# Kernel tuning notes

Hardware: AMD Instinct MI355X
Metric: run time of the kernel (lower is better)

Reference implementation:

```python
import jax, jax.numpy as jnp
import numpy as np

N_V, N_H, T, B = 1024, 512, 128, 256


def setup_inputs() -> dict:
    key = jax.random.key(0)
    k = jax.random.split(key, 3)
    v_data = (jax.random.uniform(k[0], (N_V, T, B)) < 0.5).astype(jnp.float32)  # binary visibles
    W = 0.01 * jax.random.normal(k[1], (N_H, N_V), jnp.float32)
    U = 0.01 * jax.random.normal(k[2], (N_H, N_H), jnp.float32)
    b_h = jnp.zeros((N_H,), jnp.float32)
    b_init = jnp.zeros((N_H,), jnp.float32)
    b_v = jnp.zeros((N_V,), jnp.float32)
    return {"v_data": v_data, "W": W, "U": U, "b_h": b_h, "b_init": b_init,
            "b_v": b_v, "CDk": 2}


def _sample_r_over_time(v, W, U, b_h, b_init):
    # v: (V,T,B) -> r: (H,T,B). Sequential mean-field recurrence over T
    # (RTRBM._sample_r_given_v_over_time: t=0 uses b_init and U=0, t>0 uses U,b_h).
    Wv = jnp.einsum('hv,vtb->thb', W, v)  # (T,H,B)
    r0 = jax.nn.sigmoid(Wv[0] + b_init[:, None])

    def step(r_lag, wv_t):
        r_t = jax.nn.sigmoid(wv_t + U @ r_lag + b_h[:, None])
        return r_t, r_t

    _, rs = jax.lax.scan(step, r0, Wv[1:])
    r = jnp.concatenate([r0[None], rs], axis=0)  # (T,H,B)
    return jnp.transpose(r, (1, 0, 2))  # (H,T,B)


def _parallel_r(v, r_lagged, W, U, b_h, b_init):
    # RTRBM._parallel_sample_r_h_given_v probabilities; v:(V,T,B), r_lagged:(H,T,B)
    r0 = jax.nn.sigmoid(jnp.einsum('hv,vb->hb', W, v[:, 0]) + b_init[:, None])
    rr = jax.nn.sigmoid(jnp.einsum('hv,vtb->htb', W, v[:, 1:])
                        + jnp.einsum('hr,rtb->htb', U, r_lagged[:, :-1])
                        + b_h[:, None, None])
    return jnp.concatenate([r0[:, None], rr], axis=1)  # (H,T,B)


def reference(v_data, W, U, b_h, b_init, b_v, CDk):
    key = jax.random.key(42)
    r_data = _sample_r_over_time(v_data, W, U, b_h, b_init)
    key, sk = jax.random.split(key)
    h_model = jax.random.bernoulli(sk, _parallel_r(v_data, r_data, W, U, b_h, b_init)).astype(v_data.dtype)
    for _ in range(CDk - 1):  # CD-k Gibbs chain (CDk is a concrete Python int)
        key, k1, k2 = jax.random.split(key, 3)
        v_prob = jax.nn.sigmoid(jnp.einsum('hv,htb->vtb', W, h_model) + b_v[:, None, None])
        v_model = jax.random.bernoulli(k1, v_prob).astype(v_data.dtype)
        h_model = jax.random.bernoulli(k2, _parallel_r(v_model, r_data, W, U, b_h, b_init)).astype(v_data.dtype)
    key, kf = jax.random.split(key)
    v_model = jax.random.bernoulli(
        kf, jax.nn.sigmoid(jnp.einsum('hv,htb->vtb', W, h_model) + b_v[:, None, None])
    ).astype(v_data.dtype)
    return (v_model, r_data)
```

## Files before the change

kernel.cpp:

```cpp
#include <hip/hip_runtime.h>
#include <hip/hip_bf16.h>
#include <stdint.h>

typedef unsigned long long u64;
typedef uint32_t u32;
typedef __attribute__((ext_vector_type(8))) short bf16x8;
typedef __attribute__((ext_vector_type(4))) float f32x4;

#define NV 1024
#define NH 512
#define TT 128
#define BB 256
#define TBsz (TT*BB)
#define HTBsz (NH*TBsz)
#define VTBsz (NV*TBsz)
#define NWV (NV/64)
#define NWH (NH/64)
#define QCAP 1048576u
#define DELTA 5e-4

__host__ __device__ inline void tf2x32(uint32_t k0, uint32_t k1,
                                       uint32_t x0, uint32_t x1,
                                       uint32_t& o0, uint32_t& o1) {
  const uint32_t ks2 = k0 ^ k1 ^ 0x1BD11BDAu;
#define ROTL(x,d) (((x)<<(d))|((x)>>(32-(d))))
#define RND(r) { x0 += x1; x1 = ROTL(x1,r); x1 ^= x0; }
  x0 += k0;  x1 += k1;
  RND(13) RND(15) RND(26) RND(6)
  x0 += k1;  x1 += ks2 + 1u;
  RND(17) RND(29) RND(16) RND(24)
  x0 += ks2; x1 += k0 + 2u;
  RND(13) RND(15) RND(26) RND(6)
  x0 += k0;  x1 += k1 + 3u;
  RND(17) RND(29) RND(16) RND(24)
  x0 += k1;  x1 += ks2 + 4u;
  RND(13) RND(15) RND(26) RND(6)
  x0 += ks2; x1 += k0 + 5u;
  o0 = x0; o1 = x1;
#undef RND
#undef ROTL
}

__device__ inline double tf_uniform64(uint32_t k0, uint32_t k1, uint32_t i) {
  uint32_t o0, o1;
  tf2x32(k0, k1, 0u, i, o0, o1);
  uint32_t bits = o0 ^ o1;
  uint32_t fb = (bits >> 9) | 0x3f800000u;
  float f = __uint_as_float(fb) - 1.0f;
  return (double)f;
}

__device__ inline double sigmoid64(double x) { return 1.0 / (1.0 + exp(-x)); }

__global__ __launch_bounds__(256) void kcvt(const float* __restrict__ s,
                                            double* __restrict__ d, int n) {
  int i = blockIdx.x * 256 + threadIdx.x;
  if (i < n) d[i] = (double)s[i];
}

__global__ __launch_bounds__(256) void kprepU(const float* __restrict__ U,
                                              float4* __restrict__ UB) {
  int i = blockIdx.x * 256 + threadIdx.x;
  int r4 = i / NH;
  int h  = i % NH;
  const float* __restrict__ p = U + (size_t)h*NH + r4*4;
  UB[i] = make_float4(p[0], p[1], p[2], p[3]);
}

__global__ __launch_bounds__(256) void kprepUT(const float* __restrict__ U,
                                               float* __restrict__ UT) {
  int i = blockIdx.x * 256 + threadIdx.x;
  int r = i / NH;
  int h = i % NH;
  UT[i] = U[(size_t)h*NH + r];
}

__global__ __launch_bounds__(256) void kprepA(const float* __restrict__ W,
                                              ushort* __restrict__ A1,
                                              ushort* __restrict__ A2) {
  int idx = blockIdx.x * 256 + threadIdx.x;
  int i    = idx & 7;
  int lane = (idx >> 3) & 63;
  int ks   = (idx >> 9) & 15;
  int vt   = idx >> 13;
  int h = ks*32 + ((lane >> 4) << 3) + i;
  int v = vt*16 + (lane & 15);
  float w = W[(size_t)h*NV + v];
  __hip_bfloat16 b1 = __float2bfloat16(w);
  float r = w - __bfloat162float(b1);
  __hip_bfloat16 b2 = __float2bfloat16(r);
  A1[idx] = *reinterpret_cast<ushort*>(&b1);
  A2[idx] = *reinterpret_cast<ushort*>(&b2);
}

__global__ __launch_bounds__(256) void kpack_f32(const float* __restrict__ in,
                                                 u64* __restrict__ out) {
  int tb = blockIdx.x * 256 + threadIdx.x;
  for (int w = 0; w < NWV; ++w) {
    u64 m = 0;
    #pragma unroll 8
    for (int j = 0; j < 64; ++j)
      m |= (u64)(in[(size_t)(w*64 + j)*TBsz + tb] != 0.0f ? 1 : 0) << j;
    out[(size_t)tb*NWV + w] = m;
  }
}

__global__ __launch_bounds__(256) void kWv(const u64* __restrict__ vb,
                                           const double* __restrict__ W64,
                                           double* __restrict__ WvT) {
  const int HM = 8;
  int t  = blockIdx.x / (NH/HM);
  int h0 = (blockIdx.x % (NH/HM)) * HM;
  int tb = t*BB + threadIdx.x;
  u64 m[NWV];
  #pragma unroll
  for (int w = 0; w < NWV; ++w) m[w] = vb[(size_t)tb*NWV + w];
  double acc[HM];
  #pragma unroll
  for (int i = 0; i < HM; ++i) acc[i] = 0.0;
  const double2* __restrict__ W2 = (const double2*)W64;
  for (int w = 0; w < NWV; ++w) {
    u64 mw = m[w];
    #pragma unroll 8
    for (int j2 = 0; j2 < 32; ++j2) {
      double bd0 = (double)((unsigned)((mw >> (2*j2+0)) & 1ull));
      double bd1 = (double)((unsigned)((mw >> (2*j2+1)) & 1ull));
      int vi = w*32 + j2;
      #pragma unroll
      for (int i = 0; i < HM; ++i) {
        double2 wv = W2[(size_t)(h0+i)*(NV/2) + vi];
        acc[i] = fma(bd0, wv.x, acc[i]);
        acc[i] = fma(bd1, wv.y, acc[i]);
      }
    }
  }
  #pragma unroll
  for (int i = 0; i < HM; ++i)
    WvT[(size_t)tb*NH + h0 + i] = acc[i];
}

__global__ __launch_bounds__(512) void krecur(const double* __restrict__ WvT,
                                              const float4* __restrict__ UB,
                                              const float* __restrict__ bh,
                                              const float* __restrict__ binit,
                                              double* __restrict__ rT) {
  __shared__ double rA[2][NH];
  const int b = blockIdx.x;
  const int h = threadIdx.x;
  const double bhd = (double)bh[h];
  float4 ureg[32];
  #pragma unroll
  for (int i = 0; i < 32; ++i) ureg[i] = UB[(size_t)i*NH + h];
  double p = sigmoid64(WvT[(size_t)b*NH + h] + (double)binit[h]);
  rA[0][h] = p;
  rT[(size_t)b*NH + h] = p;
  __syncthreads();
  int cur = 0;
  for (int t = 1; t < TT; ++t) {
    double acc = WvT[((size_t)t*BB + b)*NH + h];
    double a0=0, a1=0, a2=0, a3=0;
    const double2* __restrict__ rA2 = (const double2*)rA[cur];
    #pragma unroll 8
    for (int r = 0; r < 128; r += 4) {
      float4 u4 = ureg[r >> 2];
      double2 q01 = rA2[(r>>1)+0];
      double2 q23 = rA2[(r>>1)+1];
      a0 = fma((double)u4.x, q01.x, a0);
      a1 = fma((double)u4.y, q01.y, a1);
      a2 = fma((double)u4.z, q23.x, a2);
      a3 = fma((double)u4.w, q23.y, a3);
    }
    #pragma unroll 4
    for (int r = 128; r < NH; r += 4) {
      float4 u4 = UB[(size_t)(r >> 2)*NH + h];
      double2 q01 = rA2[(r>>1)+0];
      double2 q23 = rA2[(r>>1)+1];
      a0 = fma((double)u4.x, q01.x, a0);
      a1 = fma((double)u4.y, q01.y, a1);
      a2 = fma((double)u4.z, q23.x, a2);
      a3 = fma((double)u4.w, q23.y, a3);
    }
    p = sigmoid64((acc + ((a0+a1)+(a2+a3))) + bhd);
    rA[cur ^ 1][h] = p;
    rT[((size_t)t*BB + b)*NH + h] = p;
    __syncthreads();
    cur ^= 1;
  }
}

__global__ __launch_bounds__(256) void ktrans_s(const double* __restrict__ rT,
                                                float* __restrict__ out_r,
                                                uint8_t* __restrict__ hbytes,
                                                u32 k0, u32 k1) {
  __shared__ double lds[32][33];
  int t  = blockIdx.x;
  int h0 = blockIdx.y * 32;
  int b0 = blockIdx.z * 32;
  int tx = threadIdx.x & 31;
  int ty = threadIdx.x >> 5;
  #pragma unroll
  for (int i = 0; i < 4; ++i) {
    int row = ty*4 + i;
    lds[row][tx] = rT[((size_t)t*BB + b0 + row)*NH + h0 + tx];
  }
  __syncthreads();
  #pragma unroll
  for (int i = 0; i < 4; ++i) {
    int row = ty*4 + i;
    out_r[(size_t)(h0+row)*TBsz + (size_t)t*BB + b0 + tx] = (float)lds[tx][row];
  }
  if (threadIdx.x < 128) {
    int tbr = threadIdx.x >> 2;
    int bix = threadIdx.x & 3;
    int tb  = t*BB + b0 + tbr;
    unsigned byte = 0;
    #pragma unroll
    for (int j = 0; j < 8; ++j) {
      int hrel = bix*8 + j;
      double p = lds[tbr][hrel];
      double u = tf_uniform64(k0, k1, (u32)((h0 + hrel)*TBsz + tb));
      byte |= (u < p) ? (1u << j) : 0u;
    }
    hbytes[(size_t)tb*(NH/8) + (h0 >> 3) + bix] = (uint8_t)byte;
  }
}

__global__ __launch_bounds__(256) void kvisM(
    const ushort* __restrict__ A1, const ushort* __restrict__ A2,
    const float* __restrict__ bv, const u64* __restrict__ hbits,
    u64* __restrict__ vbits, float* __restrict__ vf,
    u32* __restrict__ queue, u32* __restrict__ cnt, u32 k0, u32 k1) {
  __shared__ ushort Blds[64*512];
  int nblk = blockIdx.x & 511;
  int vblk = blockIdx.x >> 9;
  int tb0 = nblk * 64, v0 = vblk * 64;
  int tid = threadIdx.x;
  {
    int c = tid >> 2, seg = tid & 3;
    const u64* hp = hbits + (size_t)(tb0 + c)*NWH + seg*2;
    #pragma unroll
    for (int half = 0; half < 2; ++half) {
      u64 mm = hp[half];
      int kbase = seg*128 + half*64;
      #pragma unroll
      for (int j2 = 0; j2 < 32; ++j2) {
        int k = kbase + 2*j2;
        u32 val = (u32)((mm >> (2*j2)) & 1ull) * 0x3F80u
                | (u32)((mm >> (2*j2+1)) & 1ull) * 0x3F800000u;
        int blk = (k >> 3) ^ (c & 7);
        *(u32*)&Blds[c*512 + (blk << 3) + (k & 7)] = val;
      }
    }
  }
  __syncthreads();
  int wv = tid >> 6, l = tid & 63;
  int wr = wv >> 1, wc = wv & 1;
  f32x4 acc[2][2];
  #pragma unroll
  for (int m = 0; m < 2; ++m)
    #pragma unroll
    for (int n = 0; n < 2; ++n) acc[m][n] = (f32x4){0.f,0.f,0.f,0.f};
  for (int ks = 0; ks < 16; ++ks) {
    bf16x8 bf[2];
    #pragma unroll
    for (int n = 0; n < 2; ++n) {
      int col = wc*32 + n*16 + (l & 15);
      int k = ks*32 + ((l >> 4) << 3);
      int blk = (k >> 3) ^ (col & 7);
      bf[n] = *(const bf16x8*)&Blds[col*512 + (blk << 3)];
    }
    #pragma unroll
    for (int m = 0; m < 2; ++m) {
      int vt = vblk*4 + wr*2 + m;
      size_t abase = (((size_t)vt*16 + ks)*64 + l)*8;
      bf16x8 a1 = *(const bf16x8*)&A1[abase];
      bf16x8 a2 = *(const bf16x8*)&A2[abase];
      #pragma unroll
      for (int n = 0; n < 2; ++n) {
        acc[m][n] = __builtin_amdgcn_mfma_f32_16x16x32_bf16(a1, bf[n], acc[m][n], 0,0,0);
        acc[m][n] = __builtin_amdgcn_mfma_f32_16x16x32_bf16(a2, bf[n], acc[m][n], 0,0,0);
      }
    }
  }
  u64 mask[2] = {0, 0};
  int coln[2];
  #pragma unroll
  for (int n = 0; n < 2; ++n) {
    int col = wc*32 + n*16 + (l & 15);
    coln[n] = col;
    int tb = tb0 + col;
    #pragma unroll
    for (int m = 0; m < 2; ++m) {
      #pragma unroll
      for (int r = 0; r < 4; ++r) {
        int vrel = wr*32 + m*16 + ((l >> 4) << 2) + r;
        int v = v0 + vrel;
        float p = 1.f / (1.f + __expf(-(acc[m][n][r] + bv[v])));
        size_t o = (size_t)v*TBsz + tb;
        double u = tf_uniform64(k0, k1, (u32)o);
        double diff = (double)p - u;
        unsigned smp = diff > 0.0 ? 1u : 0u;
        if (fabs(diff) < DELTA) {
          u32 s = atomicAdd(cnt, 1u);
          if (s < QCAP) queue[s] = (u32)o;
        }
        if (smp) mask[n] |= 1ull << vrel;
        if (vf) vf[o] = (float)smp;
      }
    }
  }
  if (vbits) {
    __syncthreads();
    u64* sbits = (u64*)Blds;
    if (tid < 64) sbits[tid] = 0;
    __syncthreads();
    atomicOr(&sbits[coln[0]], mask[0]);
    atomicOr(&sbits[coln[1]], mask[1]);
    __syncthreads();
    if (tid < 64)
      vbits[(size_t)(tb0 + tid)*NWV + (v0 >> 6)] = sbits[tid];
  }
}

__global__ __launch_bounds__(256) void kvis_fix(
    const float* __restrict__ W, const float* __restrict__ bv,
    const u64* __restrict__ hbits, u64* __restrict__ fixbits,
    float* __restrict__ vf, const u32* __restrict__ queue,
    const u32* __restrict__ cnt, u32 k0, u32 k1) {
  u32 n = *cnt; if (n > QCAP) n = QCAP;
  for (u32 q = blockIdx.x*256 + threadIdx.x; q < n; q += gridDim.x*256) {
    u32 o = queue[q];
    u32 v = o / TBsz, tb = o % TBsz;
    double a0=0, a1=0, a2=0, a3=0;
    for (int w = 0; w < NWH; ++w) {
      u64 mw = hbits[(size_t)tb*NWH + w];
      for (int j = 0; j < 64; j += 4) {
        if ((mw >> (j+0)) & 1ull) a0 += (double)W[(size_t)(w*64+j+0)*NV + v];
        if ((mw >> (j+1)) & 1ull) a1 += (double)W[(size_t)(w*64+j+1)*NV + v];
        if ((mw >> (j+2)) & 1ull) a2 += (double)W[(size_t)(w*64+j+2)*NV + v];
        if ((mw >> (j+3)) & 1ull) a3 += (double)W[(size_t)(w*64+j+3)*NV + v];
      }
    }
    double p = sigmoid64(((a0+a1)+(a2+a3)) + (double)bv[v]);
    double u = tf_uniform64(k0, k1, o);
    unsigned smp = (u < p) ? 1u : 0u;
    if (vf) vf[o] = (float)smp;
    if (fixbits) {
      size_t wi = (size_t)tb*NWV + (v >> 6);
      unsigned bit = v & 63u;
      unsigned cur = (unsigned)((fixbits[wi] >> bit) & 1ull);
      if (cur != smp) atomicXor(&fixbits[wi], 1ull << bit);
    }
  }
}

__global__ __launch_bounds__(256) void khid32(
    const u64* __restrict__ vbits, const float* __restrict__ W,
    const float* __restrict__ UT, const float* __restrict__ bh,
    const float* __restrict__ binit, const float* __restrict__ r32,
    uint8_t* __restrict__ hbytes, u32* __restrict__ queue,
    u32* __restrict__ cnt, u32 k0, u32 k1) {
  const int HM = 8;
  int t  = blockIdx.x / (NH/HM);
  int h0 = (blockIdx.x % (NH/HM)) * HM;
  int tb = t*BB + threadIdx.x;
  u64 m[NWV];
  #pragma unroll
  for (int w = 0; w < NWV; ++w) m[w] = vbits[(size_t)tb*NWV + w];
  float acc[HM];
  #pragma unroll
  for (int i = 0; i < HM; ++i) acc[i] = 0.f;
  const float4* __restrict__ W4 = (const float4*)W;
  for (int w = 0; w < NWV; ++w) {
    u64 mw = m[w];
    #pragma unroll 4
    for (int j4 = 0; j4 < 16; ++j4) {
      float bd0 = (float)((u32)((mw >> (4*j4+0)) & 1ull));
      float bd1 = (float)((u32)((mw >> (4*j4+1)) & 1ull));
      float bd2 = (float)((u32)((mw >> (4*j4+2)) & 1ull));
      float bd3 = (float)((u32)((mw >> (4*j4+3)) & 1ull));
      int vi = w*16 + j4;
      #pragma unroll
      for (int i = 0; i < HM; ++i) {
        float4 wv = W4[(size_t)(h0+i)*(NV/4) + vi];
        acc[i] = fmaf(bd0, wv.x, acc[i]);
        acc[i] = fmaf(bd1, wv.y, acc[i]);
        acc[i] = fmaf(bd2, wv.z, acc[i]);
        acc[i] = fmaf(bd3, wv.w, acc[i]);
      }
    }
  }
  if (t > 0) {
    const float* __restrict__ rp = r32 + (size_t)(t-1)*BB + threadIdx.x;
    const float4* __restrict__ UT4 = (const float4*)UT;
    #pragma unroll 4
    for (int r = 0; r < NH; ++r) {
      float rv = rp[(size_t)r*TBsz];
      float4 ua = UT4[(size_t)r*(NH/4) + (h0 >> 2) + 0];
      float4 ub = UT4[(size_t)r*(NH/4) + (h0 >> 2) + 1];
      acc[0] = fmaf(ua.x, rv, acc[0]);
      acc[1] = fmaf(ua.y, rv, acc[1]);
      acc[2] = fmaf(ua.z, rv, acc[2]);
      acc[3] = fmaf(ua.w, rv, acc[3]);
      acc[4] = fmaf(ub.x, rv, acc[4]);
      acc[5] = fmaf(ub.y, rv, acc[5]);
      acc[6] = fmaf(ub.z, rv, acc[6]);
      acc[7] = fmaf(ub.w, rv, acc[7]);
    }
    #pragma unroll
    for (int i = 0; i < HM; ++i) acc[i] += bh[h0+i];
  } else {
    #pragma unroll
    for (int i = 0; i < HM; ++i) acc[i] += binit[h0+i];
  }
  unsigned byte = 0;
  #pragma unroll
  for (int i = 0; i < HM; ++i) {
    float p = 1.f / (1.f + __expf(-acc[i]));
    size_t o = (size_t)(h0+i)*TBsz + tb;
    double u = tf_uniform64(k0, k1, (u32)o);
    double diff = (double)p - u;
    unsigned smp = diff > 0.0 ? 1u : 0u;
    if (fabs(diff) < DELTA) {
      u32 s = atomicAdd(cnt, 1u);
      if (s < QCAP) queue[s] = (u32)o;
    }
    byte |= smp << i;
  }
  hbytes[(size_t)tb*(NH/8) + (h0 >> 3)] = (uint8_t)byte;
}

__global__ __launch_bounds__(256) void khid_fix(
    const u64* __restrict__ vbits, const float* __restrict__ W,
    const double* __restrict__ U64, const float* __restrict__ bh,
    const float* __restrict__ binit, const double* __restrict__ rT,
    u64* __restrict__ fixbits, const u32* __restrict__ queue,
    const u32* __restrict__ cnt, u32 k0, u32 k1) {
  u32 n = *cnt; if (n > QCAP) n = QCAP;
  for (u32 q = blockIdx.x*256 + threadIdx.x; q < n; q += gridDim.x*256) {
    u32 o = queue[q];
    u32 h = o / TBsz, tb = o % TBsz;
    u32 t = tb / BB, b = tb % BB;
    double a0=0, a1=0, a2=0, a3=0;
    for (int w = 0; w < NWV; ++w) {
      u64 mw = vbits[(size_t)tb*NWV + w];
      for (int j = 0; j < 64; j += 4) {
        if ((mw >> (j+0)) & 1ull) a0 += (double)W[(size_t)h*NV + w*64+j+0];
        if ((mw >> (j+1)) & 1ull) a1 += (double)W[(size_t)h*NV + w*64+j+1];
        if ((mw >> (j+2)) & 1ull) a2 += (double)W[(size_t)h*NV + w*64+j+2];
        if ((mw >> (j+3)) & 1ull) a3 += (double)W[(size_t)h*NV + w*64+j+3];
      }
    }
    double logit = (a0+a1) + (a2+a3);
    if (t > 0) {
      const double* __restrict__ rp = rT + ((size_t)(t-1)*BB + b)*NH;
      const double* __restrict__ Ur = U64 + (size_t)h*NH;
      double u0=0, u1=0, u2=0, u3=0;
      for (int r = 0; r < NH; r += 4) {
        u0 = fma(Ur[r+0], rp[r+0], u0);
        u1 = fma(Ur[r+1], rp[r+1], u1);
        u2 = fma(Ur[r+2], rp[r+2], u2);
        u3 = fma(Ur[r+3], rp[r+3], u3);
      }
      logit = (logit + ((u0+u1)+(u2+u3))) + (double)bh[h];
    } else {
      logit += (double)binit[h];
    }
    double p = sigmoid64(logit);
    double u = tf_uniform64(k0, k1, o);
    unsigned smp = (u < p) ? 1u : 0u;
    size_t wi = (size_t)tb*NWH + (h >> 6);
    unsigned bit = h & 63u;
    unsigned cur = (unsigned)((fixbits[wi] >> bit) & 1ull);
    if (cur != smp) atomicXor(&fixbits[wi], 1ull << bit);
  }
}

extern "C" void kernel_launch(void* const* d_in, const int* in_sizes, int n_in,
                              void* d_out, int out_size, void* d_ws, size_t ws_size,
                              hipStream_t stream) {
  const float* vd    = (const float*)d_in[0];
  const float* W     = (const float*)d_in[1];
  const float* U     = (const float*)d_in[2];
  const float* bh    = (const float*)d_in[3];
  const float* binit = (const float*)d_in[4];
  const float* bv    = (const float*)d_in[5];

  float* out_v = (float*)d_out;
  float* out_r = (float*)d_out + VTBsz;
  double* WvT = (double*)d_out;

  char* w = (char*)d_ws;
  double* rT    = (double*)w;  w += (size_t)HTBsz*8;
  u64* vdbits   = (u64*)w;     w += (size_t)TBsz*NWV*8;
  u64* v1bits   = (u64*)w;     w += (size_t)TBsz*NWV*8;
  u64* h1bits   = (u64*)w;     w += (size_t)TBsz*NWH*8;
  u64* h2bits   = (u64*)w;     w += (size_t)TBsz*NWH*8;
  double* W64   = (double*)w;  w += (size_t)NH*NV*8;
  double* U64   = (double*)w;  w += (size_t)NH*NH*8;
  float4* UB    = (float4*)w;  w += (size_t)NH*NH*4;
  float* UT     = (float*)w;   w += (size_t)NH*NH*4;
  ushort* A1    = (ushort*)w;  w += (size_t)NH*NV*2;
  ushort* A2    = (ushort*)w;  w += (size_t)NH*NV*2;
  u32* q0       = (u32*)w;     w += (size_t)QCAP*4;
  u32* q1       = (u32*)w;     w += (size_t)QCAP*4;
  u32* q2       = (u32*)w;     w += (size_t)QCAP*4;
  u32* cnt      = (u32*)w;     w += 256;
  (void)ws_size; (void)in_sizes; (void)n_in; (void)out_size;

  uint32_t ka0,ka1, sk0,sk1;
  tf2x32(0u,42u, 0u,0u, ka0,ka1);
  tf2x32(0u,42u, 0u,1u, sk0,sk1);
  uint32_t kb0,kb1, k10,k11, k20,k21;
  tf2x32(ka0,ka1, 0u,0u, kb0,kb1);
  tf2x32(ka0,ka1, 0u,1u, k10,k11);
  tf2x32(ka0,ka1, 0u,2u, k20,k21);
  uint32_t kc0,kc1, kf0,kf1;
  tf2x32(kb0,kb1, 0u,0u, kc0,kc1);
  tf2x32(kb0,kb1, 0u,1u, kf0,kf1);

  hipMemsetAsync(cnt, 0, 3*sizeof(u32), stream);

  kcvt<<<(NH*NV+255)/256, 256, 0, stream>>>(W, W64, NH*NV);
  kcvt<<<(NH*NH+255)/256, 256, 0, stream>>>(U, U64, NH*NH);
  kprepU<<<(NH*NH/4)/256, 256, 0, stream>>>(U, UB);
  kprepUT<<<(NH*NH)/256, 256, 0, stream>>>(U, UT);
  kprepA<<<(NH*NV)/256, 256, 0, stream>>>(W, A1, A2);
  kpack_f32<<<TBsz/256, 256, 0, stream>>>(vd, vdbits);

  kWv<<<TT*(NH/8), 256, 0, stream>>>(vdbits, W64, WvT);

  krecur<<<BB, NH, 0, stream>>>(WvT, UB, bh, binit, rT);

  ktrans_s<<<dim3(TT, NH/32, BB/32), 256, 0, stream>>>(rT, out_r,
                                                       (uint8_t*)h1bits, sk0, sk1);

  kvisM<<<16*512, 256, 0, stream>>>(A1, A2, bv, h1bits, v1bits, nullptr,
                                    q0, cnt+0, k10, k11);
  kvis_fix<<<128, 256, 0, stream>>>(W, bv, h1bits, v1bits, nullptr,
                                    q0, cnt+0, k10, k11);

  khid32<<<TT*(NH/8), 256, 0, stream>>>(v1bits, W, UT, bh, binit, out_r,
                                        (uint8_t*)h2bits, q1, cnt+1, k20, k21);
  khid_fix<<<128, 256, 0, stream>>>(v1bits, W, U64, bh, binit, rT,
                                    h2bits, q1, cnt+1, k20, k21);

  kvisM<<<16*512, 256, 0, stream>>>(A1, A2, bv, h2bits, nullptr, out_v,
                                    q2, cnt+2, kf0, kf1);
  kvis_fix<<<128, 256, 0, stream>>>(W, bv, h2bits, nullptr, out_v,
                                    q2, cnt+2, kf0, kf1);
}
```

Before: 5.709 ms.

## Compute second hidden sampling pass with bf16 split-precision MFMA GEMM

```diff
diff --git a/kernel.cpp b/kernel.cpp
--- a/kernel.cpp
+++ b/kernel.cpp
@@ -67,14 +67,6 @@
   UB[i] = make_float4(p[0], p[1], p[2], p[3]);
 }
 
-__global__ __launch_bounds__(256) void kprepUT(const float* __restrict__ U,
-                                               float* __restrict__ UT) {
-  int i = blockIdx.x * 256 + threadIdx.x;
-  int r = i / NH;
-  int h = i % NH;
-  UT[i] = U[(size_t)h*NH + r];
-}
-
 __global__ __launch_bounds__(256) void kprepA(const float* __restrict__ W,
                                               ushort* __restrict__ A1,
                                               ushort* __restrict__ A2) {
@@ -93,6 +85,42 @@
   A2[idx] = *reinterpret_cast<ushort*>(&b2);
 }
 
+__global__ __launch_bounds__(256) void kprepAW(const float* __restrict__ W,
+                                               ushort* __restrict__ AW1,
+                                               ushort* __restrict__ AW2) {
+  int idx = blockIdx.x * 256 + threadIdx.x;
+  int i    = idx & 7;
+  int lane = (idx >> 3) & 63;
+  int kt   = (idx >> 9) & 31;
+  int ht   = idx >> 14;
+  int h = ht*16 + (lane & 15);
+  int v = kt*32 + ((lane >> 4) << 3) + i;
+  float w = W[(size_t)h*NV + v];
+  __hip_bfloat16 b1 = __float2bfloat16(w);
+  float r = w - __bfloat162float(b1);
+  __hip_bfloat16 b2 = __float2bfloat16(r);
+  AW1[idx] = *reinterpret_cast<ushort*>(&b1);
+  AW2[idx] = *reinterpret_cast<ushort*>(&b2);
+}
+
+__global__ __launch_bounds__(256) void kprepAU(const float* __restrict__ U,
+                                               ushort* __restrict__ AU1,
+                                               ushort* __restrict__ AU2) {
+  int idx = blockIdx.x * 256 + threadIdx.x;
+  int i    = idx & 7;
+  int lane = (idx >> 3) & 63;
+  int kt   = (idx >> 9) & 15;
+  int ht   = idx >> 13;
+  int h = ht*16 + (lane & 15);
+  int r = kt*32 + ((lane >> 4) << 3) + i;
+  float u = U[(size_t)h*NH + r];
+  __hip_bfloat16 b1 = __float2bfloat16(u);
+  float rs = u - __bfloat162float(b1);
+  __hip_bfloat16 b2 = __float2bfloat16(rs);
+  AU1[idx] = *reinterpret_cast<ushort*>(&b1);
+  AU2[idx] = *reinterpret_cast<ushort*>(&b2);
+}
+
 __global__ __launch_bounds__(256) void kpack_f32(const float* __restrict__ in,
                                                  u64* __restrict__ out) {
   int tb = blockIdx.x * 256 + threadIdx.x;
@@ -148,9 +176,6 @@
   const int b = blockIdx.x;
   const int h = threadIdx.x;
   const double bhd = (double)bh[h];
-  float4 ureg[32];
-  #pragma unroll
-  for (int i = 0; i < 32; ++i) ureg[i] = UB[(size_t)i*NH + h];
   double p = sigmoid64(WvT[(size_t)b*NH + h] + (double)binit[h]);
   rA[0][h] = p;
   rT[(size_t)b*NH + h] = p;
@@ -160,18 +185,8 @@
     double acc = WvT[((size_t)t*BB + b)*NH + h];
     double a0=0, a1=0, a2=0, a3=0;
     const double2* __restrict__ rA2 = (const double2*)rA[cur];
-    #pragma unroll 8
-    for (int r = 0; r < 128; r += 4) {
-      float4 u4 = ureg[r >> 2];
-      double2 q01 = rA2[(r>>1)+0];
-      double2 q23 = rA2[(r>>1)+1];
-      a0 = fma((double)u4.x, q01.x, a0);
-      a1 = fma((double)u4.y, q01.y, a1);
-      a2 = fma((double)u4.z, q23.x, a2);
-      a3 = fma((double)u4.w, q23.y, a3);
-    }
     #pragma unroll 4
-    for (int r = 128; r < NH; r += 4) {
+    for (int r = 0; r < NH; r += 4) {
       float4 u4 = UB[(size_t)(r >> 2)*NH + h];
       double2 q01 = rA2[(r>>1)+0];
       double2 q23 = rA2[(r>>1)+1];
@@ -320,6 +335,159 @@
     if (tid < 64)
       vbits[(size_t)(tb0 + tid)*NWV + (v0 >> 6)] = sbits[tid];
   }
+}
+
+__global__ __launch_bounds__(256) void khidM(
+    const ushort* __restrict__ AW1, const ushort* __restrict__ AW2,
+    const ushort* __restrict__ AU1, const ushort* __restrict__ AU2,
+    const float* __restrict__ bh, const float* __restrict__ binit,
+    const u64* __restrict__ vbits, const float* __restrict__ r32,
+    u64* __restrict__ h2bits, u32* __restrict__ queue,
+    u32* __restrict__ cnt, u32 k0, u32 k1) {
+  __shared__ ushort Blds[64*512];
+  int nblk = blockIdx.x & 511;
+  int hblk = blockIdx.x >> 9;
+  int tb0 = nblk * 64, h0 = hblk * 64;
+  int t = tb0 >> 8;
+  int tid = threadIdx.x;
+  int wv = tid >> 6, l = tid & 63;
+  int wr = wv >> 1, wc = wv & 1;
+  f32x4 acc[2][2];
+  #pragma unroll
+  for (int m = 0; m < 2; ++m)
+    #pragma unroll
+    for (int n = 0; n < 2; ++n) acc[m][n] = (f32x4){0.f,0.f,0.f,0.f};
+
+  for (int q = 0; q < 2; ++q) {
+    {
+      int c = tid >> 2, seg = tid & 3;
+      const u64* vp = vbits + (size_t)(tb0 + c)*NWV + q*8 + seg*2;
+      #pragma unroll
+      for (int half = 0; half < 2; ++half) {
+        u64 mm = vp[half];
+        int kbase = seg*128 + half*64;
+        #pragma unroll
+        for (int j2 = 0; j2 < 32; ++j2) {
+          int k = kbase + 2*j2;
+          u32 val = (u32)((mm >> (2*j2)) & 1ull) * 0x3F80u
+                  | (u32)((mm >> (2*j2+1)) & 1ull) * 0x3F800000u;
+          int blk = (k >> 3) ^ (c & 7);
+          *(u32*)&Blds[c*512 + (blk << 3) + (k & 7)] = val;
+        }
+      }
+    }
+    __syncthreads();
+    for (int ks = 0; ks < 16; ++ks) {
+      int kt = q*16 + ks;
+      bf16x8 bf[2];
+      #pragma unroll
+      for (int n = 0; n < 2; ++n) {
+        int col = wc*32 + n*16 + (l & 15);
+        int k = ks*32 + ((l >> 4) << 3);
+        int blk = (k >> 3) ^ (col & 7);
+        bf[n] = *(const bf16x8*)&Blds[col*512 + (blk << 3)];
+      }
+      #pragma unroll
+      for (int m = 0; m < 2; ++m) {
+        int ht = hblk*4 + wr*2 + m;
+        size_t abase = (((size_t)ht*32 + kt)*64 + l)*8;
+        bf16x8 a1 = *(const bf16x8*)&AW1[abase];
+        bf16x8 a2 = *(const bf16x8*)&AW2[abase];
+        #pragma unroll
+        for (int n = 0; n < 2; ++n) {
+          acc[m][n] = __builtin_amdgcn_mfma_f32_16x16x32_bf16(a1, bf[n], acc[m][n], 0,0,0);
+          acc[m][n] = __builtin_amdgcn_mfma_f32_16x16x32_bf16(a2, bf[n], acc[m][n], 0,0,0);
+        }
+      }
+    }
+    __syncthreads();
+  }
+
+  if (t > 0) {
+    int tbl0 = tb0 - 256;
+    for (int pl = 0; pl < 2; ++pl) {
+      {
+        int c = tid >> 2, rseg = tid & 3;
+        const float* rp = r32 + tbl0 + c;
+        for (int rr = 0; rr < 128; ++rr) {
+          int r = rseg*128 + rr;
+          float x = rp[(size_t)r*TBsz];
+          __hip_bfloat16 b1 = __float2bfloat16(x);
+          ushort ub;
+          if (pl == 0) {
+            ub = *reinterpret_cast<ushort*>(&b1);
+          } else {
+            float res = x - __bfloat162float(b1);
+            __hip_bfloat16 b2 = __float2bfloat16(res);
+            ub = *reinterpret_cast<ushort*>(&b2);
+          }
+          int blk = (r >> 3) ^ (c & 7);
+          Blds[c*512 + (blk << 3) + (r & 7)] = ub;
+        }
+      }
+      __syncthreads();
+      for (int ks = 0; ks < 16; ++ks) {
+        bf16x8 bf[2];
+        #pragma unroll
+        for (int n = 0; n < 2; ++n) {
+          int col = wc*32 + n*16 + (l & 15);
+          int k = ks*32 + ((l >> 4) << 3);
+          int blk = (k >> 3) ^ (col & 7);
+          bf[n] = *(const bf16x8*)&Blds[col*512 + (blk << 3)];
+        }
+        #pragma unroll
+        for (int m = 0; m < 2; ++m) {
+          int ht = hblk*4 + wr*2 + m;
+          size_t abase = (((size_t)ht*16 + ks)*64 + l)*8;
+          bf16x8 a1 = *(const bf16x8*)&AU1[abase];
+          bf16x8 a2 = *(const bf16x8*)&AU2[abase];
+          #pragma unroll
+          for (int n = 0; n < 2; ++n) {
+            acc[m][n] = __builtin_amdgcn_mfma_f32_16x16x32_bf16(a1, bf[n], acc[m][n], 0,0,0);
+            acc[m][n] = __builtin_amdgcn_mfma_f32_16x16x32_bf16(a2, bf[n], acc[m][n], 0,0,0);
+          }
+        }
+      }
+      __syncthreads();
+    }
+  }
+
+  const float* __restrict__ bias = (t > 0) ? bh : binit;
+  u64 mask[2] = {0, 0};
+  int coln[2];
+  #pragma unroll
+  for (int n = 0; n < 2; ++n) {
+    int col = wc*32 + n*16 + (l & 15);
+    coln[n] = col;
+    int tb = tb0 + col;
+    #pragma unroll
+    for (int m = 0; m < 2; ++m) {
+      #pragma unroll
+      for (int r = 0; r < 4; ++r) {
+        int hrel = wr*32 + m*16 + ((l >> 4) << 2) + r;
+        int h = h0 + hrel;
+        float p = 1.f / (1.f + __expf(-(acc[m][n][r] + bias[h])));
+        size_t o = (size_t)h*TBsz + tb;
+        double u = tf_uniform64(k0, k1, (u32)o);
+        double diff = (double)p - u;
+        unsigned smp = diff > 0.0 ? 1u : 0u;
+        if (fabs(diff) < DELTA) {
+          u32 s = atomicAdd(cnt, 1u);
+          if (s < QCAP) queue[s] = (u32)o;
+        }
+        if (smp) mask[n] |= 1ull << hrel;
+      }
+    }
+  }
+  __syncthreads();
+  u64* sbits = (u64*)Blds;
+  if (tid < 64) sbits[tid] = 0;
+  __syncthreads();
+  atomicOr(&sbits[coln[0]], mask[0]);
+  atomicOr(&sbits[coln[1]], mask[1]);
+  __syncthreads();
+  if (tid < 64)
+    h2bits[(size_t)(tb0 + tid)*NWH + hblk] = sbits[tid];
 }
 
 __global__ __launch_bounds__(256) void kvis_fix(
@@ -352,82 +520,6 @@
       if (cur != smp) atomicXor(&fixbits[wi], 1ull << bit);
     }
   }
-}
-
-__global__ __launch_bounds__(256) void khid32(
-    const u64* __restrict__ vbits, const float* __restrict__ W,
-    const float* __restrict__ UT, const float* __restrict__ bh,
-    const float* __restrict__ binit, const float* __restrict__ r32,
-    uint8_t* __restrict__ hbytes, u32* __restrict__ queue,
-    u32* __restrict__ cnt, u32 k0, u32 k1) {
-  const int HM = 8;
-  int t  = blockIdx.x / (NH/HM);
-  int h0 = (blockIdx.x % (NH/HM)) * HM;
-  int tb = t*BB + threadIdx.x;
-  u64 m[NWV];
-  #pragma unroll
-  for (int w = 0; w < NWV; ++w) m[w] = vbits[(size_t)tb*NWV + w];
-  float acc[HM];
-  #pragma unroll
-  for (int i = 0; i < HM; ++i) acc[i] = 0.f;
-  const float4* __restrict__ W4 = (const float4*)W;
-  for (int w = 0; w < NWV; ++w) {
-    u64 mw = m[w];
-    #pragma unroll 4
-    for (int j4 = 0; j4 < 16; ++j4) {
-      float bd0 = (float)((u32)((mw >> (4*j4+0)) & 1ull));
-      float bd1 = (float)((u32)((mw >> (4*j4+1)) & 1ull));
-      float bd2 = (float)((u32)((mw >> (4*j4+2)) & 1ull));
-      float bd3 = (float)((u32)((mw >> (4*j4+3)) & 1ull));
-      int vi = w*16 + j4;
-      #pragma unroll
-      for (int i = 0; i < HM; ++i) {
-        float4 wv = W4[(size_t)(h0+i)*(NV/4) + vi];
-        acc[i] = fmaf(bd0, wv.x, acc[i]);
-        acc[i] = fmaf(bd1, wv.y, acc[i]);
-        acc[i] = fmaf(bd2, wv.z, acc[i]);
-        acc[i] = fmaf(bd3, wv.w, acc[i]);
-      }
-    }
-  }
-  if (t > 0) {
-    const float* __restrict__ rp = r32 + (size_t)(t-1)*BB + threadIdx.x;
-    const float4* __restrict__ UT4 = (const float4*)UT;
-    #pragma unroll 4
-    for (int r = 0; r < NH; ++r) {
-      float rv = rp[(size_t)r*TBsz];
-      float4 ua = UT4[(size_t)r*(NH/4) + (h0 >> 2) + 0];
-      float4 ub = UT4[(size_t)r*(NH/4) + (h0 >> 2) + 1];
-      acc[0] = fmaf(ua.x, rv, acc[0]);
-      acc[1] = fmaf(ua.y, rv, acc[1]);
-      acc[2] = fmaf(ua.z, rv, acc[2]);
-      acc[3] = fmaf(ua.w, rv, acc[3]);
-      acc[4] = fmaf(ub.x, rv, acc[4]);
-      acc[5] = fmaf(ub.y, rv, acc[5]);
-      acc[6] = fmaf(ub.z, rv, acc[6]);
-      acc[7] = fmaf(ub.w, rv, acc[7]);
-    }
-    #pragma unroll
-    for (int i = 0; i < HM; ++i) acc[i] += bh[h0+i];
-  } else {
-    #pragma unroll
-    for (int i = 0; i < HM; ++i) acc[i] += binit[h0+i];
-  }
-  unsigned byte = 0;
-  #pragma unroll
-  for (int i = 0; i < HM; ++i) {
-    float p = 1.f / (1.f + __expf(-acc[i]));
-    size_t o = (size_t)(h0+i)*TBsz + tb;
-    double u = tf_uniform64(k0, k1, (u32)o);
-    double diff = (double)p - u;
-    unsigned smp = diff > 0.0 ? 1u : 0u;
-    if (fabs(diff) < DELTA) {
-      u32 s = atomicAdd(cnt, 1u);
-      if (s < QCAP) queue[s] = (u32)o;
-    }
-    byte |= smp << i;
-  }
-  hbytes[(size_t)tb*(NH/8) + (h0 >> 3)] = (uint8_t)byte;
 }
 
 __global__ __launch_bounds__(256) void khid_fix(
@@ -499,9 +591,12 @@
   double* W64   = (double*)w;  w += (size_t)NH*NV*8;
   double* U64   = (double*)w;  w += (size_t)NH*NH*8;
   float4* UB    = (float4*)w;  w += (size_t)NH*NH*4;
-  float* UT     = (float*)w;   w += (size_t)NH*NH*4;
   ushort* A1    = (ushort*)w;  w += (size_t)NH*NV*2;
   ushort* A2    = (ushort*)w;  w += (size_t)NH*NV*2;
+  ushort* AW1   = (ushort*)w;  w += (size_t)NH*NV*2;
+  ushort* AW2   = (ushort*)w;  w += (size_t)NH*NV*2;
+  ushort* AU1   = (ushort*)w;  w += (size_t)NH*NH*2;
+  ushort* AU2   = (ushort*)w;  w += (size_t)NH*NH*2;
   u32* q0       = (u32*)w;     w += (size_t)QCAP*4;
   u32* q1       = (u32*)w;     w += (size_t)QCAP*4;
   u32* q2       = (u32*)w;     w += (size_t)QCAP*4;
@@ -524,8 +619,9 @@
   kcvt<<<(NH*NV+255)/256, 256, 0, stream>>>(W, W64, NH*NV);
   kcvt<<<(NH*NH+255)/256, 256, 0, stream>>>(U, U64, NH*NH);
   kprepU<<<(NH*NH/4)/256, 256, 0, stream>>>(U, UB);
-  kprepUT<<<(NH*NH)/256, 256, 0, stream>>>(U, UT);
   kprepA<<<(NH*NV)/256, 256, 0, stream>>>(W, A1, A2);
+  kprepAW<<<(NH*NV)/256, 256, 0, stream>>>(W, AW1, AW2);
+  kprepAU<<<(NH*NH)/256, 256, 0, stream>>>(U, AU1, AU2);
   kpack_f32<<<TBsz/256, 256, 0, stream>>>(vd, vdbits);
 
   kWv<<<TT*(NH/8), 256, 0, stream>>>(vdbits, W64, WvT);
@@ -540,8 +636,8 @@
   kvis_fix<<<128, 256, 0, stream>>>(W, bv, h1bits, v1bits, nullptr,
                                     q0, cnt+0, k10, k11);
 
-  khid32<<<TT*(NH/8), 256, 0, stream>>>(v1bits, W, UT, bh, binit, out_r,
-                                        (uint8_t*)h2bits, q1, cnt+1, k20, k21);
+  khidM<<<8*512, 256, 0, stream>>>(AW1, AW2, AU1, AU2, bh, binit,
+                                   v1bits, out_r, h2bits, q1, cnt+1, k20, k21);
   khid_fix<<<128, 256, 0, stream>>>(v1bits, W, U64, bh, binit, rT,
                                     h2bits, q1, cnt+1, k20, k21);
 
```

Result: faster. 5.023 ms (-12.0%).
